# Optimization experiments

Measured on AMD Instinct MI355X. Metric: run time of the kernel, lower is better.

The kernel has to match this reference:

```python
import jax, jax.numpy as jnp
import numpy as np


def euler_xyz_to_matrix(angles):
    # pytorch3d euler_angles_to_matrix(angles, 'XYZ') = R_X(a0) @ R_Y(a1) @ R_Z(a2)
    ax, ay, az = angles[..., 0], angles[..., 1], angles[..., 2]
    cx, sx = jnp.cos(ax), jnp.sin(ax)
    cy, sy = jnp.cos(ay), jnp.sin(ay)
    cz, sz = jnp.cos(az), jnp.sin(az)
    one = jnp.ones_like(ax)
    zero = jnp.zeros_like(ax)
    Rx = jnp.stack([one, zero, zero, zero, cx, -sx, zero, sx, cx], axis=-1).reshape(*ax.shape, 3, 3)
    Ry = jnp.stack([cy, zero, sy, zero, one, zero, -sy, zero, cy], axis=-1).reshape(*ax.shape, 3, 3)
    Rz = jnp.stack([cz, -sz, zero, sz, cz, zero, zero, zero, one], axis=-1).reshape(*ax.shape, 3, 3)
    return Rx @ Ry @ Rz


def chamfer_bidir(x, y):
    # x, y: [R, I, N, 3]. Squared-distance chamfer, mean point reduction, per (R,I) batch.
    x2 = jnp.sum(x * x, axis=-1)  # [R,I,N]
    y2 = jnp.sum(y * y, axis=-1)  # [R,I,N]
    # d2[r,i,n,m] = |x_n - y_m|^2
    d2 = x2[..., :, None] + y2[..., None, :] - 2.0 * jnp.einsum('rind,rimd->rinm', x, y)
    cham_x = jnp.mean(jnp.min(d2, axis=-1), axis=-1)  # x -> nearest y
    cham_y = jnp.mean(jnp.min(d2, axis=-2), axis=-1)  # y -> nearest x
    return cham_x + cham_y  # [R, I]


def setup_inputs() -> dict:
    key = jax.random.key(0)
    k1, k2, k3, k4 = jax.random.split(key, 4)
    R, I, N = 4, 16, 2048
    source_points = jax.random.normal(k1, (R, I, N, 3), dtype=jnp.float32)
    target_points = jax.random.normal(k2, (I, N, 3), dtype=jnp.float32)
    rotation = 0.1 * jax.random.normal(k3, (R, I, 3), dtype=jnp.float32)
    translation = 0.1 * jax.random.normal(k4, (R, I, 3), dtype=jnp.float32)
    scale = jnp.ones((R, I), dtype=jnp.float32)
    return {
        'source_points': source_points,
        'target_points': target_points,
        'rotation': rotation,
        'translation': translation,
        'scale': scale,
    }


def reference(source_points, target_points, rotation, translation, scale):
    R, I, N, _ = source_points.shape
    rot = euler_xyz_to_matrix(rotation)  # [R,I,3,3]
    # Transform per original: 4x4 matrix with rows [:3,:] scaled by `scale`,
    # so p' = scale * (rot @ p + translation).
    transformed = scale[..., None, None] * (
        jnp.einsum('rind,rikd->rink', source_points, rot) + translation[..., None, :]
    )  # [R,I,N,3]
    # target_points [I,N,3] broadcast to [R,I,N,3] (original repeats along R)
    target = jnp.broadcast_to(target_points[None], transformed.shape)
    # original calls chamfer_distance(target, transformed): x=target, y=transformed
    return chamfer_bidir(target, transformed)  # [R, I]
```

## Files before the change

kernel.cpp:

```cpp
#include <hip/hip_runtime.h>
#include <math.h>

#define RDIM 4
#define IDIM 16
#define NPAIR 64
#define NPTS 2048
#define THREADS 256
#define ROWSB 256
#define RBLK (NPTS / ROWSB)
#define TILES (NPTS / 32)
#define SCRS 68
#define ONEBF 0x3F80u

typedef __attribute__((ext_vector_type(8))) short bf16x8;
typedef __attribute__((ext_vector_type(16))) float f32x16;
typedef __attribute__((ext_vector_type(4))) float f32x4;

__device__ __forceinline__ unsigned int f2bf(float f) {
    union { float f; unsigned int u; } v; v.f = f;
    return (v.u + 0x7FFFu + ((v.u >> 16) & 1u)) >> 16;
}
__device__ __forceinline__ float bf2f(unsigned int h) {
    union { unsigned int u; float f; } v; v.u = h << 16; return v.f;
}

__device__ __forceinline__ void make_rot(const float* __restrict__ rotv, int pair,
                                         float& r00, float& r01, float& r02,
                                         float& r10, float& r11, float& r12,
                                         float& r20, float& r21, float& r22) {
    const float ax = rotv[pair * 3 + 0];
    const float ay = rotv[pair * 3 + 1];
    const float az = rotv[pair * 3 + 2];
    float sx, cx, sy, cy, sz, cz;
    sincosf(ax, &sx, &cx);
    sincosf(ay, &sy, &cy);
    sincosf(az, &sz, &cz);
    r00 = cy * cz;                r01 = -cy * sz;               r02 = sy;
    r10 = cx * sz + sx * sy * cz; r11 = cx * cz - sx * sy * sz; r12 = -sx * cy;
    r20 = sx * sz - cx * sy * cz; r21 = sx * cz + cx * sy * sz; r22 = cx * cy;
}

__device__ __forceinline__ uint4 brec(float v0, float v1, float v2) {
    const float b0 = -2.0f * v0, b1 = -2.0f * v1, b2 = -2.0f * v2;
    const unsigned int h0 = f2bf(b0), h1 = f2bf(b1), h2 = f2bf(b2);
    const unsigned int l0 = f2bf(b0 - bf2f(h0));
    const unsigned int l1 = f2bf(b1 - bf2f(h1));
    const unsigned int l2 = f2bf(b2 - bf2f(h2));
    const float n2 = v0 * v0 + v1 * v1 + v2 * v2;
    const unsigned int nh = f2bf(n2), nl = f2bf(n2 - bf2f(nh));
    return make_uint4(h0 | (h1 << 16), h2 | (l0 << 16), l1 | (l2 << 16), nh | (nl << 16));
}
__device__ __forceinline__ void arec(float q0, float q1, float q2, uint4& a0, uint4& a1) {
    const unsigned int h0 = f2bf(q0), h1 = f2bf(q1), h2 = f2bf(q2);
    const unsigned int l0 = f2bf(q0 - bf2f(h0));
    const unsigned int l1 = f2bf(q1 - bf2f(h1));
    const unsigned int l2 = f2bf(q2 - bf2f(h2));
    a0 = make_uint4(h0 | (h1 << 16), h2 | (l0 << 16), l1 | (l2 << 16), ONEBF);
    a1 = make_uint4(l0 | (l1 << 16), l2 | (h0 << 16), h1 | (h2 << 16), ONEBF << 16);
}

__global__ __launch_bounds__(THREADS)
void prep(const float* __restrict__ src, const float* __restrict__ tgt,
          const float* __restrict__ rotv, const float* __restrict__ trav,
          const float* __restrict__ scal,
          uint4* __restrict__ Yb, uint4* __restrict__ Ya,
          uint4* __restrict__ Xb, uint4* __restrict__ Xa)
{
    const int b = blockIdx.x;
    const int tid = threadIdx.x;
    if (b < NPAIR) {
        const int pair = b;
        float r00, r01, r02, r10, r11, r12, r20, r21, r22;
        make_rot(rotv, pair, r00, r01, r02, r10, r11, r12, r20, r21, r22);
        const float t0 = trav[pair * 3 + 0];
        const float t1 = trav[pair * 3 + 1];
        const float t2 = trav[pair * 3 + 2];
        const float s  = scal[pair];
        const float* __restrict__ srcp = src + (size_t)pair * NPTS * 3;
#pragma unroll
        for (int u = 0; u < NPTS / THREADS; ++u) {
            const int m = u * THREADS + tid;
            const float p0 = srcp[m * 3 + 0];
            const float p1 = srcp[m * 3 + 1];
            const float p2 = srcp[m * 3 + 2];
            const float y0 = s * fmaf(r00, p0, fmaf(r01, p1, fmaf(r02, p2, t0)));
            const float y1 = s * fmaf(r10, p0, fmaf(r11, p1, fmaf(r12, p2, t1)));
            const float y2 = s * fmaf(r20, p0, fmaf(r21, p1, fmaf(r22, p2, t2)));
            Yb[(size_t)pair * NPTS + m] = brec(y0, y1, y2);
            uint4 a0, a1;
            arec(y0, y1, y2, a0, a1);
            Ya[((size_t)pair * NPTS + m) * 2 + 0] = a0;
            Ya[((size_t)pair * NPTS + m) * 2 + 1] = a1;
        }
    } else {
        const int i = b - NPAIR;
        const float* __restrict__ tgtp = tgt + (size_t)i * NPTS * 3;
#pragma unroll
        for (int u = 0; u < NPTS / THREADS; ++u) {
            const int m = u * THREADS + tid;
            const float x0 = tgtp[m * 3 + 0];
            const float x1 = tgtp[m * 3 + 1];
            const float x2 = tgtp[m * 3 + 2];
            Xb[(size_t)i * NPTS + m] = brec(x0, x1, x2);
            uint4 a0, a1;
            arec(x0, x1, x2, a0, a1);
            Xa[((size_t)i * NPTS + m) * 2 + 0] = a0;
            Xa[((size_t)i * NPTS + m) * 2 + 1] = a1;
        }
    }
}

__global__ __launch_bounds__(THREADS, 3)
void chamfer_main(const uint4* __restrict__ Yb, const uint4* __restrict__ Ya,
                  const uint4* __restrict__ Xb, const uint4* __restrict__ Xa,
                  float* __restrict__ out)
{
    __shared__ alignas(16) unsigned char smem[34816 + 8192];
    __shared__ float wsum[4];
    unsigned short* sB = (unsigned short*)smem;
    float* scratch = (float*)smem;
    unsigned short* sA = (unsigned short*)(smem + 34816);

    const int pair  = blockIdx.x;
    const int rb    = blockIdx.y;
    const int passB = blockIdx.z;
    const int i     = pair & (IDIM - 1);
    const int tid   = threadIdx.x;
    const int lane  = tid & 63;
    const int w     = tid >> 6;
    const int c31   = lane & 31;
    const int h     = lane >> 5;

    const uint4* __restrict__ gB = (passB == 0) ? (Yb + (size_t)pair * NPTS)
                                                : (Xb + (size_t)i * NPTS);
    const uint4* __restrict__ gA = (passB == 0)
        ? (Xa + ((size_t)i * NPTS + rb * ROWSB) * 2)
        : (Ya + ((size_t)pair * NPTS + rb * ROWSB) * 2);

#pragma unroll
    for (int j = 0; j < 8; ++j)
        ((uint4*)sB)[j * THREADS + tid] = gB[j * THREADS + tid];
    ((uint4*)sA)[tid] = gA[tid];
    ((uint4*)sA)[THREADS + tid] = gA[THREADS + tid];
    __syncthreads();

    bf16x8 af[2];
    af[0] = *(const bf16x8*)&sA[(w * 64 + c31) * 16 + h * 8];
    af[1] = *(const bf16x8*)&sA[(w * 64 + 32 + c31) * 16 + h * 8];

    float mn[2][16];
#pragma unroll
    for (int rt = 0; rt < 2; ++rt)
#pragma unroll
        for (int j = 0; j < 16; ++j) mn[rt][j] = 3.4e38f;

    const f32x16 zero16 = {0,0,0,0, 0,0,0,0, 0,0,0,0, 0,0,0,0};

#pragma unroll 4
    for (int t = 0; t < TILES; ++t) {
        const bf16x8 bf = *(const bf16x8*)&sB[(t * 32 + c31) * 8];
        const f32x16 d0 = __builtin_amdgcn_mfma_f32_32x32x16_bf16(af[0], bf, zero16, 0, 0, 0);
        const f32x16 d1 = __builtin_amdgcn_mfma_f32_32x32x16_bf16(af[1], bf, zero16, 0, 0, 0);
#pragma unroll
        for (int j = 0; j < 16; ++j) {
            mn[0][j] = fminf(mn[0][j], d0[j]);
            mn[1][j] = fminf(mn[1][j], d1[j]);
        }
    }
    __syncthreads();

#pragma unroll
    for (int rt = 0; rt < 2; ++rt)
#pragma unroll
        for (int g2 = 0; g2 < 4; ++g2) {
            const int rowb = rt * 32 + 8 * g2 + 4 * h;
            f32x4 v4;
            v4[0] = mn[rt][g2 * 4 + 0];
            v4[1] = mn[rt][g2 * 4 + 1];
            v4[2] = mn[rt][g2 * 4 + 2];
            v4[3] = mn[rt][g2 * 4 + 3];
            *(f32x4*)&scratch[(w * 32 + c31) * SCRS + rowb] = v4;
        }
    __syncthreads();

    float m = scratch[(w * 32) * SCRS + lane];
#pragma unroll
    for (int c = 1; c < 32; ++c)
        m = fminf(m, scratch[(w * 32 + c) * SCRS + lane]);

    const unsigned short* ar = &sA[tid * 16];
    const float q0 = bf2f(ar[0]) + bf2f(ar[3]);
    const float q1 = bf2f(ar[1]) + bf2f(ar[4]);
    const float q2 = bf2f(ar[2]) + bf2f(ar[5]);
    float v = m + q0 * q0 + q1 * q1 + q2 * q2;

#pragma unroll
    for (int off = 32; off > 0; off >>= 1)
        v += __shfl_down(v, off, 64);
    if (lane == 0) wsum[w] = v;
    __syncthreads();
    if (tid == 0) {
        const float tot = wsum[0] + wsum[1] + wsum[2] + wsum[3];
        atomicAdd(&out[pair], tot * (1.0f / NPTS));
    }
}

extern "C" void kernel_launch(void* const* d_in, const int* in_sizes, int n_in,
                              void* d_out, int out_size, void* d_ws, size_t ws_size,
                              hipStream_t stream) {
    const float* src  = (const float*)d_in[0];
    const float* tgt  = (const float*)d_in[1];
    const float* rotv = (const float*)d_in[2];
    const float* trav = (const float*)d_in[3];
    const float* scal = (const float*)d_in[4];
    float* out = (float*)d_out;

    char* ws = (char*)d_ws;
    uint4* Yb = (uint4*)ws;
    uint4* Ya = (uint4*)(ws + (size_t)NPAIR * NPTS * 16);
    uint4* Xb = (uint4*)(ws + (size_t)NPAIR * NPTS * 48);
    uint4* Xa = (uint4*)(ws + (size_t)NPAIR * NPTS * 48 + (size_t)IDIM * NPTS * 16);

    hipMemsetAsync(out, 0, NPAIR * sizeof(float), stream);

    prep<<<NPAIR + IDIM, THREADS, 0, stream>>>(src, tgt, rotv, trav, scal, Yb, Ya, Xb, Xa);

    dim3 grid(NPAIR, RBLK, 2);
    chamfer_main<<<grid, THREADS, 0, stream>>>(Yb, Ya, Xb, Xa, out);
}
```

Baseline: 84.86 us.

## Compute A-side split-bf16 operands in main kernel instead of prep workspace

The prep kernel no longer writes the 32-byte-per-point A-operand records (Ya/Xa). The main kernel recomputes the rotated/transformed row points directly from the raw inputs, builds the hi/lo bf16 A fragments into shared memory, and stores the exact fp32 squared norm for the final sum. This cuts workspace writes and reads at the cost of recomputing sincos and the transform per block. The tile loop also processes two B tiles per iteration with paired fminf.

After: 98.77 us. 16.4% more time.

```diff
diff --git a/kernel.cpp b/kernel.cpp
--- a/kernel.cpp
+++ b/kernel.cpp
@@ -15,6 +15,7 @@
 typedef __attribute__((ext_vector_type(8))) short bf16x8;
 typedef __attribute__((ext_vector_type(16))) float f32x16;
 typedef __attribute__((ext_vector_type(4))) float f32x4;
+
 
 __device__ __forceinline__ unsigned int f2bf(float f) {
     union { float f; unsigned int u; } v; v.f = f;
@@ -50,21 +51,12 @@
     const unsigned int nh = f2bf(n2), nl = f2bf(n2 - bf2f(nh));
     return make_uint4(h0 | (h1 << 16), h2 | (l0 << 16), l1 | (l2 << 16), nh | (nl << 16));
 }
-__device__ __forceinline__ void arec(float q0, float q1, float q2, uint4& a0, uint4& a1) {
-    const unsigned int h0 = f2bf(q0), h1 = f2bf(q1), h2 = f2bf(q2);
-    const unsigned int l0 = f2bf(q0 - bf2f(h0));
-    const unsigned int l1 = f2bf(q1 - bf2f(h1));
-    const unsigned int l2 = f2bf(q2 - bf2f(h2));
-    a0 = make_uint4(h0 | (h1 << 16), h2 | (l0 << 16), l1 | (l2 << 16), ONEBF);
-    a1 = make_uint4(l0 | (l1 << 16), l2 | (h0 << 16), h1 | (h2 << 16), ONEBF << 16);
-}
 
 __global__ __launch_bounds__(THREADS)
 void prep(const float* __restrict__ src, const float* __restrict__ tgt,
           const float* __restrict__ rotv, const float* __restrict__ trav,
           const float* __restrict__ scal,
-          uint4* __restrict__ Yb, uint4* __restrict__ Ya,
-          uint4* __restrict__ Xb, uint4* __restrict__ Xa)
+          uint4* __restrict__ Yb, uint4* __restrict__ Xb)
 {
     const int b = blockIdx.x;
     const int tid = threadIdx.x;
@@ -87,10 +79,6 @@
             const float y1 = s * fmaf(r10, p0, fmaf(r11, p1, fmaf(r12, p2, t1)));
             const float y2 = s * fmaf(r20, p0, fmaf(r21, p1, fmaf(r22, p2, t2)));
             Yb[(size_t)pair * NPTS + m] = brec(y0, y1, y2);
-            uint4 a0, a1;
-            arec(y0, y1, y2, a0, a1);
-            Ya[((size_t)pair * NPTS + m) * 2 + 0] = a0;
-            Ya[((size_t)pair * NPTS + m) * 2 + 1] = a1;
         }
     } else {
         const int i = b - NPAIR;
@@ -98,24 +86,20 @@
 #pragma unroll
         for (int u = 0; u < NPTS / THREADS; ++u) {
             const int m = u * THREADS + tid;
-            const float x0 = tgtp[m * 3 + 0];
-            const float x1 = tgtp[m * 3 + 1];
-            const float x2 = tgtp[m * 3 + 2];
-            Xb[(size_t)i * NPTS + m] = brec(x0, x1, x2);
-            uint4 a0, a1;
-            arec(x0, x1, x2, a0, a1);
-            Xa[((size_t)i * NPTS + m) * 2 + 0] = a0;
-            Xa[((size_t)i * NPTS + m) * 2 + 1] = a1;
+            Xb[(size_t)i * NPTS + m] = brec(tgtp[m * 3 + 0], tgtp[m * 3 + 1], tgtp[m * 3 + 2]);
         }
     }
 }
 
 __global__ __launch_bounds__(THREADS, 3)
-void chamfer_main(const uint4* __restrict__ Yb, const uint4* __restrict__ Ya,
-                  const uint4* __restrict__ Xb, const uint4* __restrict__ Xa,
+void chamfer_main(const float* __restrict__ src, const float* __restrict__ tgt,
+                  const float* __restrict__ rotv, const float* __restrict__ trav,
+                  const float* __restrict__ scal,
+                  const uint4* __restrict__ Yb, const uint4* __restrict__ Xb,
                   float* __restrict__ out)
 {
     __shared__ alignas(16) unsigned char smem[34816 + 8192];
+    __shared__ float rowq2[ROWSB];
     __shared__ float wsum[4];
     unsigned short* sB = (unsigned short*)smem;
     float* scratch = (float*)smem;
@@ -133,66 +117,85 @@
 
     const uint4* __restrict__ gB = (passB == 0) ? (Yb + (size_t)pair * NPTS)
                                                 : (Xb + (size_t)i * NPTS);
-    const uint4* __restrict__ gA = (passB == 0)
-        ? (Xa + ((size_t)i * NPTS + rb * ROWSB) * 2)
-        : (Ya + ((size_t)pair * NPTS + rb * ROWSB) * 2);
-
 #pragma unroll
     for (int j = 0; j < 8; ++j)
         ((uint4*)sB)[j * THREADS + tid] = gB[j * THREADS + tid];
-    ((uint4*)sA)[tid] = gA[tid];
-    ((uint4*)sA)[THREADS + tid] = gA[THREADS + tid];
-    __syncthreads();
-
-    bf16x8 af[2];
-    af[0] = *(const bf16x8*)&sA[(w * 64 + c31) * 16 + h * 8];
-    af[1] = *(const bf16x8*)&sA[(w * 64 + 32 + c31) * 16 + h * 8];
-
-    float mn[2][16];
-#pragma unroll
-    for (int rt = 0; rt < 2; ++rt)
-#pragma unroll
-        for (int j = 0; j < 16; ++j) mn[rt][j] = 3.4e38f;
+
+    {
+        const int n = rb * ROWSB + tid;
+        float q0, q1, q2v;
+        if (passB == 0) {
+            const float* __restrict__ tgtp = tgt + (size_t)i * NPTS * 3;
+            q0 = tgtp[n * 3 + 0]; q1 = tgtp[n * 3 + 1]; q2v = tgtp[n * 3 + 2];
+        } else {
+            float r00, r01, r02, r10, r11, r12, r20, r21, r22;
+            make_rot(rotv, pair, r00, r01, r02, r10, r11, r12, r20, r21, r22);
+            const float t0 = trav[pair * 3 + 0];
+            const float t1 = trav[pair * 3 + 1];
+            const float t2 = trav[pair * 3 + 2];
+            const float s  = scal[pair];
+            const float* __restrict__ srcp = src + (size_t)pair * NPTS * 3;
+            const float p0 = srcp[n * 3 + 0];
+            const float p1 = srcp[n * 3 + 1];
+            const float p2 = srcp[n * 3 + 2];
+            q0  = s * fmaf(r00, p0, fmaf(r01, p1, fmaf(r02, p2, t0)));
+            q1  = s * fmaf(r10, p0, fmaf(r11, p1, fmaf(r12, p2, t1)));
+            q2v = s * fmaf(r20, p0, fmaf(r21, p1, fmaf(r22, p2, t2)));
+        }
+        rowq2[tid] = q0 * q0 + q1 * q1 + q2v * q2v;
+        const unsigned int h0 = f2bf(q0), h1 = f2bf(q1), h2 = f2bf(q2v);
+        const unsigned int l0 = f2bf(q0 - bf2f(h0));
+        const unsigned int l1 = f2bf(q1 - bf2f(h1));
+        const unsigned int l2 = f2bf(q2v - bf2f(h2));
+        uint4* rk = (uint4*)&sA[tid * 16];
+        rk[0] = make_uint4(h0 | (h1 << 16), h2 | (l0 << 16), l1 | (l2 << 16), ONEBF);
+        rk[1] = make_uint4(l0 | (l1 << 16), l2 | (h0 << 16), h1 | (h2 << 16), ONEBF << 16);
+    }
+    __syncthreads();
+
+    bf16x8 af0 = *(const bf16x8*)&sA[(w * 64 + c31) * 16 + h * 8];
+    bf16x8 af1 = *(const bf16x8*)&sA[(w * 64 + 32 + c31) * 16 + h * 8];
+
+    float mn0[16], mn1[16];
+#pragma unroll
+    for (int j = 0; j < 16; ++j) { mn0[j] = 3.4e38f; mn1[j] = 3.4e38f; }
 
     const f32x16 zero16 = {0,0,0,0, 0,0,0,0, 0,0,0,0, 0,0,0,0};
 
-#pragma unroll 4
-    for (int t = 0; t < TILES; ++t) {
-        const bf16x8 bf = *(const bf16x8*)&sB[(t * 32 + c31) * 8];
-        const f32x16 d0 = __builtin_amdgcn_mfma_f32_32x32x16_bf16(af[0], bf, zero16, 0, 0, 0);
-        const f32x16 d1 = __builtin_amdgcn_mfma_f32_32x32x16_bf16(af[1], bf, zero16, 0, 0, 0);
-#pragma unroll
-        for (int j = 0; j < 16; ++j) {
-            mn[0][j] = fminf(mn[0][j], d0[j]);
-            mn[1][j] = fminf(mn[1][j], d1[j]);
-        }
-    }
-    __syncthreads();
-
-#pragma unroll
-    for (int rt = 0; rt < 2; ++rt)
-#pragma unroll
-        for (int g2 = 0; g2 < 4; ++g2) {
-            const int rowb = rt * 32 + 8 * g2 + 4 * h;
-            f32x4 v4;
-            v4[0] = mn[rt][g2 * 4 + 0];
-            v4[1] = mn[rt][g2 * 4 + 1];
-            v4[2] = mn[rt][g2 * 4 + 2];
-            v4[3] = mn[rt][g2 * 4 + 3];
-            *(f32x4*)&scratch[(w * 32 + c31) * SCRS + rowb] = v4;
-        }
+#pragma unroll 2
+    for (int t2 = 0; t2 < TILES / 2; ++t2) {
+        const bf16x8 bfA = *(const bf16x8*)&sB[((t2 * 2 + 0) * 32 + c31) * 8];
+        const bf16x8 bfB = *(const bf16x8*)&sB[((t2 * 2 + 1) * 32 + c31) * 8];
+        const f32x16 d0a = __builtin_amdgcn_mfma_f32_32x32x16_bf16(af0, bfA, zero16, 0, 0, 0);
+        const f32x16 d0b = __builtin_amdgcn_mfma_f32_32x32x16_bf16(af0, bfB, zero16, 0, 0, 0);
+#pragma unroll
+        for (int j = 0; j < 16; ++j)
+            mn0[j] = fminf(mn0[j], fminf(d0a[j], d0b[j]));
+        const f32x16 d1a = __builtin_amdgcn_mfma_f32_32x32x16_bf16(af1, bfA, zero16, 0, 0, 0);
+        const f32x16 d1b = __builtin_amdgcn_mfma_f32_32x32x16_bf16(af1, bfB, zero16, 0, 0, 0);
+#pragma unroll
+        for (int j = 0; j < 16; ++j)
+            mn1[j] = fminf(mn1[j], fminf(d1a[j], d1b[j]));
+    }
+    __syncthreads();
+
+#pragma unroll
+    for (int g2 = 0; g2 < 4; ++g2) {
+        f32x4 v4;
+        v4[0] = mn0[g2 * 4 + 0]; v4[1] = mn0[g2 * 4 + 1];
+        v4[2] = mn0[g2 * 4 + 2]; v4[3] = mn0[g2 * 4 + 3];
+        *(f32x4*)&scratch[(w * 32 + c31) * SCRS + 8 * g2 + 4 * h] = v4;
+        v4[0] = mn1[g2 * 4 + 0]; v4[1] = mn1[g2 * 4 + 1];
+        v4[2] = mn1[g2 * 4 + 2]; v4[3] = mn1[g2 * 4 + 3];
+        *(f32x4*)&scratch[(w * 32 + c31) * SCRS + 32 + 8 * g2 + 4 * h] = v4;
+    }
     __syncthreads();
 
     float m = scratch[(w * 32) * SCRS + lane];
 #pragma unroll
     for (int c = 1; c < 32; ++c)
         m = fminf(m, scratch[(w * 32 + c) * SCRS + lane]);
-
-    const unsigned short* ar = &sA[tid * 16];
-    const float q0 = bf2f(ar[0]) + bf2f(ar[3]);
-    const float q1 = bf2f(ar[1]) + bf2f(ar[4]);
-    const float q2 = bf2f(ar[2]) + bf2f(ar[5]);
-    float v = m + q0 * q0 + q1 * q1 + q2 * q2;
+    float v = m + rowq2[tid];
 
 #pragma unroll
     for (int off = 32; off > 0; off >>= 1)
@@ -217,14 +220,12 @@
 
     char* ws = (char*)d_ws;
     uint4* Yb = (uint4*)ws;
-    uint4* Ya = (uint4*)(ws + (size_t)NPAIR * NPTS * 16);
-    uint4* Xb = (uint4*)(ws + (size_t)NPAIR * NPTS * 48);
-    uint4* Xa = (uint4*)(ws + (size_t)NPAIR * NPTS * 48 + (size_t)IDIM * NPTS * 16);
+    uint4* Xb = (uint4*)(ws + (size_t)NPAIR * NPTS * 16);
 
     hipMemsetAsync(out, 0, NPAIR * sizeof(float), stream);
 
-    prep<<<NPAIR + IDIM, THREADS, 0, stream>>>(src, tgt, rotv, trav, scal, Yb, Ya, Xb, Xa);
+    prep<<<NPAIR + IDIM, THREADS, 0, stream>>>(src, tgt, rotv, trav, scal, Yb, Xb);
 
     dim3 grid(NPAIR, RBLK, 2);
-    chamfer_main<<<grid, THREADS, 0, stream>>>(Yb, Ya, Xb, Xa, out);
-}
+    chamfer_main<<<grid, THREADS, 0, stream>>>(src, tgt, rotv, trav, scal, Yb, Xb, out);
+}
```
